# Performance work log

Hardware: AMD Instinct MI355X
Metric: run time of the kernel (lower is better)

## Reference

```python
import jax, jax.numpy as jnp
import numpy as np
import math

N = 100000
E = 1600000
D = 256          # input_size
H = 64           # head_size = input_size // n_heads = 256 // 4


def setup_inputs() -> dict:
    key = jax.random.key(0)
    k1, k2, k3, k4, k5 = jax.random.split(key, 5)
    X = jax.random.normal(k1, (N, D), dtype=jnp.float32)
    edge_index = jax.random.randint(k2, (2, E), 0, N, dtype=jnp.int64)
    # Linear(input_size, head_size, bias=False) weights, stored as [D, H] so Q = X @ Wq
    s = 1.0 / math.sqrt(D)
    Wq = jax.random.uniform(k3, (D, H), dtype=jnp.float32, minval=-s, maxval=s)
    Wk = jax.random.uniform(k4, (D, H), dtype=jnp.float32, minval=-s, maxval=s)
    Wv = jax.random.uniform(k5, (D, H), dtype=jnp.float32, minval=-s, maxval=s)
    return {"X": X, "Wq": Wq, "Wk": Wk, "Wv": Wv, "edge_index": edge_index}


def reference(X, Wq, Wk, Wv, edge_index):
    dk = math.sqrt(H)
    Q = X @ Wq  # [N, H]
    K = X @ Wk
    V = X @ Wv
    src = edge_index[0]  # row of sparse matrix -> softmax segment (dim=1 softmax)
    dst = edge_index[1]  # column -> neighbor supplying K/V
    scores = jnp.sum(Q[src] * K[dst], axis=-1) / dk  # [E]
    # per-row (per src node) stable softmax over edges
    m = jax.ops.segment_max(scores, src, num_segments=N)          # [N], -inf for empty rows
    m = jnp.where(jnp.isfinite(m), m, 0.0)
    e = jnp.exp(scores - m[src])                                   # [E]
    denom = jax.ops.segment_sum(e, src, num_segments=N)            # [N]
    alpha = e / jnp.maximum(denom[src], 1e-38)                     # [E]
    # scatter-weighted V aggregation: out[i] = sum_{(i,j) in edges} alpha_ij * V[j]
    out = jax.ops.segment_sum(alpha[:, None] * V[dst], src, num_segments=N)  # [N, H]
    return out
```

## Files before the change

### kernel.cpp

```cpp
#include <hip/hip_runtime.h>

typedef unsigned short u16;
typedef unsigned int u32;
typedef short short8 __attribute__((ext_vector_type(8)));
typedef float f32x4 __attribute__((ext_vector_type(4)));
typedef u32 u32x4 __attribute__((ext_vector_type(4)));

__device__ __forceinline__ u16 f2bf(float f) {
    union { float f; u32 i; } c; c.f = f;
    u32 i = c.i;
    return (u16)((i + 0x7FFFu + ((i >> 16) & 1u)) >> 16);
}
__device__ __forceinline__ float bf2f(u16 u) {
    union { u32 i; float f; } c; c.i = ((u32)u) << 16; return c.f;
}
__device__ __forceinline__ void bf2x(u32 p, float& lo, float& hi) {
    union { u32 i; float f; } a, b;
    a.i = p << 16; b.i = p & 0xFFFF0000u;
    lo = a.f; hi = b.f;
}
__device__ __forceinline__ u32 cvtpk_bf16(float lo, float hi) {
    u32 r;
    asm("v_cvt_pk_bf16_f32 %0, %1, %2" : "=v"(r) : "v"(lo), "v"(hi));
    return r;
}

__global__ void wfrag_kernel(const float* __restrict__ Wq,
                             const float* __restrict__ Wk,
                             const float* __restrict__ Wv,
                             u16* __restrict__ wf)
{
    int idx = blockIdx.x * 256 + threadIdx.x;
    if (idx >= 12 * 8 * 64) return;
    int lane = idx & 63;
    int s = (idx >> 6) & 7;
    int t = idx >> 9;
    int n = t * 16 + (lane & 15);
    const float* Wsrc = (n < 64) ? Wq : ((n < 128) ? Wk : Wv);
    int col = n & 63;
    int kbase = s * 32 + (lane >> 4) * 8;
    u16 o[8];
#pragma unroll
    for (int j = 0; j < 8; ++j) o[j] = f2bf(Wsrc[(size_t)(kbase + j) * 64 + col]);
    *(short8*)(wf + (size_t)idx * 8) = *(const short8*)o;
}

#define TM 32
__global__ __launch_bounds__(256, 2) void qkv_mfma(
    const float* __restrict__ X, const u16* __restrict__ wf,
    float* __restrict__ Qs, u16* __restrict__ KVsb,
    int N, int NT)
{
    __shared__ float xs[TM * 256];

    const int tid  = threadIdx.x;
    const int lane = tid & 63;
    const int wave = tid >> 6;
    const int m    = lane & 15;
    const int quad = lane >> 4;
    const int t0   = wave * 3;

    const short8* wfp = (const short8*)wf;
    short8 bfr0[8], bfr1[8], bfr2[8];
#pragma unroll
    for (int s = 0; s < 8; ++s) {
        bfr0[s] = wfp[(size_t)((t0 + 0) * 8 + s) * 64 + lane];
        bfr1[s] = wfp[(size_t)((t0 + 1) * 8 + s) * 64 + lane];
        bfr2[s] = wfp[(size_t)((t0 + 2) * 8 + s) * 64 + lane];
    }

    for (int tile = blockIdx.x; tile < NT; tile += gridDim.x) {
#pragma unroll
        for (int it = 0; it < 8; ++it) {
            int c0  = (it * 4 + wave) * 64;
            int c   = c0 + lane;
            int row = c >> 6;
            int sblk = (c & 63) ^ (row & 7);
            int arow = tile * TM + row;
            if (arow >= N) arow = N - 1;
            const float* g = X + (size_t)arow * 256 + sblk * 4;
            float* l = xs + c0 * 4;
            __builtin_amdgcn_global_load_lds(
                (const __attribute__((address_space(1))) void*)g,
                (__attribute__((address_space(3))) void*)l, 16, 0, 0);
        }
        __syncthreads();

        f32x4 acc[2][3];
#pragma unroll
        for (int rb = 0; rb < 2; ++rb)
#pragma unroll
            for (int tt = 0; tt < 3; ++tt) acc[rb][tt] = (f32x4)0.f;

#pragma unroll
        for (int rb = 0; rb < 2; ++rb) {
            const int row = rb * 16 + m;
            const float* xrow = xs + row * 256;
            const int sw = m & 7;
#pragma unroll
            for (int s = 0; s < 8; ++s) {
                int B0 = quad * 2 + s * 8;
                float4 a0 = *(const float4*)(xrow + ((B0)     ^ sw) * 4);
                float4 a1 = *(const float4*)(xrow + ((B0 + 1) ^ sw) * 4);
                union { u32x4 u; short8 s8; } af;
                af.u.x = cvtpk_bf16(a0.x, a0.y);
                af.u.y = cvtpk_bf16(a0.z, a0.w);
                af.u.z = cvtpk_bf16(a1.x, a1.y);
                af.u.w = cvtpk_bf16(a1.z, a1.w);
                acc[rb][0] = __builtin_amdgcn_mfma_f32_16x16x32_bf16(af.s8, bfr0[s], acc[rb][0], 0, 0, 0);
                acc[rb][1] = __builtin_amdgcn_mfma_f32_16x16x32_bf16(af.s8, bfr1[s], acc[rb][1], 0, 0, 0);
                acc[rb][2] = __builtin_amdgcn_mfma_f32_16x16x32_bf16(af.s8, bfr2[s], acc[rb][2], 0, 0, 0);
            }
        }

#pragma unroll
        for (int rb = 0; rb < 2; ++rb) {
            int rbase = tile * TM + rb * 16 + quad * 4;
#pragma unroll
            for (int tt = 0; tt < 3; ++tt) {
                int t = t0 + tt;
                int col = (t & 3) * 16 + m;
#pragma unroll
                for (int r = 0; r < 4; ++r) {
                    int rr = rbase + r;
                    if (rr >= N) continue;
                    float v = acc[rb][tt][r];
                    if (t < 4)      Qs  [(size_t)rr * 64  + col]      = v;
                    else if (t < 8) KVsb[(size_t)rr * 128 + col]      = f2bf(v);
                    else            KVsb[(size_t)rr * 128 + 64 + col] = f2bf(v);
                }
            }
        }
        __syncthreads();
    }
}


__global__ __launch_bounds__(256) void count_kernel(
    const int* __restrict__ src, int* __restrict__ bsize,
    int E, int N, int NB, int chunk)
{
    __shared__ int cnt[512];
    for (int i = threadIdx.x; i < 512; i += 256) cnt[i] = 0;
    __syncthreads();
    int lo = blockIdx.x * chunk;
    int hi = min(E, lo + chunk);
    for (int e = lo + (int)threadIdx.x; e < hi; e += 256) {
        int s = src[e];
        if ((unsigned)s < (unsigned)N) atomicAdd(&cnt[s >> 8], 1);
    }
    __syncthreads();
    for (int b = threadIdx.x; b < NB; b += 256)
        if (cnt[b]) atomicAdd(&bsize[b], cnt[b]);
}

__global__ __launch_bounds__(512) void scan391_kernel(
    const int* __restrict__ bsize, int* __restrict__ bbase,
    int* __restrict__ cursor, int* __restrict__ row_ptr_N, int NB)
{
    __shared__ int sd[512];
    int t = threadIdx.x;
    int v = (t < NB) ? bsize[t] : 0;
    sd[t] = v;
    __syncthreads();
    for (int off = 1; off < 512; off <<= 1) {
        int x = (t >= off) ? sd[t - off] : 0;
        __syncthreads();
        sd[t] += x;
        __syncthreads();
    }
    if (t < NB) {
        int excl = sd[t] - v;
        bbase[t] = excl;
        cursor[t] = excl;
        if (t == NB - 1) {
            bbase[NB] = sd[t];
            *row_ptr_N = sd[t];
        }
    }
}

__global__ __launch_bounds__(256) void scatter_pairs_kernel(
    const int* __restrict__ src, const int* __restrict__ dst,
    int* __restrict__ cursor, int2* __restrict__ pairs,
    int E, int N, int NB, int chunk)
{
    __shared__ int cnt[512];
    __shared__ int basei[512];
    for (int i = threadIdx.x; i < 512; i += 256) cnt[i] = 0;
    __syncthreads();
    int lo = blockIdx.x * chunk;
    int hi = min(E, lo + chunk);
    for (int e = lo + (int)threadIdx.x; e < hi; e += 256) {
        int s = src[e];
        if ((unsigned)s < (unsigned)N) atomicAdd(&cnt[s >> 8], 1);
    }
    __syncthreads();
    for (int b = threadIdx.x; b < NB; b += 256)
        basei[b] = cnt[b] ? atomicAdd(&cursor[b], cnt[b]) : 0;
    __syncthreads();
    for (int i = threadIdx.x; i < 512; i += 256) cnt[i] = 0;
    __syncthreads();
    for (int e = lo + (int)threadIdx.x; e < hi; e += 256) {
        int s = src[e];
        if ((unsigned)s >= (unsigned)N) continue;
        int d = dst[e];
        if ((unsigned)d >= (unsigned)N) d = 0;
        int bk = s >> 8;
        int p = basei[bk] + atomicAdd(&cnt[bk], 1);
        pairs[p] = make_int2(s, d);
    }
}

#define MAXB 6144
__global__ __launch_bounds__(256) void sort_bucket_kernel(
    const int2* __restrict__ pairs, const int* __restrict__ bbase,
    int* __restrict__ row_ptr, int* __restrict__ sorted_dst, int N)
{
    __shared__ int deg[256];
    __shared__ int off[256];
    __shared__ int cur[256];
    __shared__ int ldst[MAXB];

    int bk = blockIdx.x;
    int n0 = bk * 256;
    int nn = min(256, N - n0);
    int base = bbase[bk];
    int size = bbase[bk + 1] - base;
    int t = threadIdx.x;

    deg[t] = 0;
    __syncthreads();
    for (int i = t; i < size; i += 256)
        atomicAdd(&deg[pairs[base + i].x & 255], 1);
    __syncthreads();
    off[t] = deg[t];
    __syncthreads();
    for (int s = 1; s < 256; s <<= 1) {
        int x = (t >= s) ? off[t - s] : 0;
        __syncthreads();
        off[t] += x;
        __syncthreads();
    }
    int excl = off[t] - deg[t];
    cur[t] = excl;
    if (t < nn) row_ptr[n0 + t] = base + excl;
    __syncthreads();
    int cap = min(size, MAXB);
    for (int i = t; i < size; i += 256) {
        int2 pr = pairs[base + i];
        int p = atomicAdd(&cur[pr.x & 255], 1);
        if (p < MAXB) ldst[p] = pr.y;
    }
    __syncthreads();
    for (int i = t; i < cap; i += 256)
        sorted_dst[base + i] = ldst[i];
    for (int i = cap + t; i < size; i += 256)
        sorted_dst[base + i] = 0;
}

__global__ __launch_bounds__(256) void attn_csr(
    const float* __restrict__ Qs, const u16* __restrict__ KVsb,
    const int* __restrict__ row_ptr, const int* __restrict__ sdst,
    float* __restrict__ out, int N)
{
    int sg = (int)((blockIdx.x * 256 + threadIdx.x) >> 3);
    if (sg >= N) return;
    int sl = threadIdx.x & 7;

    const float* qp = Qs + (size_t)sg * 64 + sl * 8;
    float4 q0 = *(const float4*)(qp);
    float4 q1 = *(const float4*)(qp + 4);

    int beg = row_ptr[sg];
    int end = row_ptr[sg + 1];

    float l = 0.f;
    float a0 = 0.f, a1 = 0.f, a2 = 0.f, a3 = 0.f;
    float a4 = 0.f, a5 = 0.f, a6 = 0.f, a7 = 0.f;

    if (beg < end) {
        int d0 = sdst[beg];
        const u16* kv = KVsb + (size_t)d0 * 128 + sl * 8;
        uint4 kr = *(const uint4*)(kv);
        uint4 vr = *(const uint4*)(kv + 64);

        for (int j = beg; j < end; ++j) {
            int jn = j + 1;
            int dn = (jn < end) ? sdst[jn] : d0;
            const u16* kvn = KVsb + (size_t)dn * 128 + sl * 8;
            uint4 krn = *(const uint4*)(kvn);
            uint4 vrn = *(const uint4*)(kvn + 64);

            float k0, k1, k2, k3, k4, k5, k6, k7;
            bf2x(kr.x, k0, k1); bf2x(kr.y, k2, k3);
            bf2x(kr.z, k4, k5); bf2x(kr.w, k6, k7);

            float p = q0.x * k0 + q0.y * k1 + q0.z * k2 + q0.w * k3
                    + q1.x * k4 + q1.y * k5 + q1.z * k6 + q1.w * k7;
            p += __shfl_xor(p, 1);
            p += __shfl_xor(p, 2);
            p += __shfl_xor(p, 4);

            float pe = __expf(p * 0.125f);

            float v0, v1, v2, v3, v4, v5, v6, v7;
            bf2x(vr.x, v0, v1); bf2x(vr.y, v2, v3);
            bf2x(vr.z, v4, v5); bf2x(vr.w, v6, v7);

            l += pe;
            a0 += pe * v0; a1 += pe * v1; a2 += pe * v2; a3 += pe * v3;
            a4 += pe * v4; a5 += pe * v5; a6 += pe * v6; a7 += pe * v7;

            kr = krn; vr = vrn;
        }
    }

    float inv = (l > 0.f) ? (1.f / l) : 0.f;
    float* op = out + (size_t)sg * 64 + sl * 8;
    *(float4*)(op)     = make_float4(a0 * inv, a1 * inv, a2 * inv, a3 * inv);
    *(float4*)(op + 4) = make_float4(a4 * inv, a5 * inv, a6 * inv, a7 * inv);
}

extern "C" void kernel_launch(void* const* d_in, const int* in_sizes, int n_in,
                              void* d_out, int out_size, void* d_ws, size_t ws_size,
                              hipStream_t stream)
{
    const float* X  = (const float*)d_in[0];
    const float* Wq = (const float*)d_in[1];
    const float* Wk = (const float*)d_in[2];
    const float* Wv = (const float*)d_in[3];
    const int*   ei = (const int*)d_in[4];

    const int N = in_sizes[0] / 256;
    const int E = in_sizes[4] / 2;
    const int* src = ei;
    const int* dst = ei + E;
    const int NB = (N + 255) >> 8;

    char* w = (char*)d_ws;
    float* Qs = (float*)w;      w += (size_t)N * 64 * sizeof(float);
    u16* KVsb = (u16*)w;        w += (size_t)N * 128 * sizeof(u16);
    int2* pairs = (int2*)w;     w += (size_t)E * sizeof(int2);
    int* sorted_dst = (int*)w;  w += (size_t)E * sizeof(int);
    int* row_ptr = (int*)w;     w += (size_t)(N + 1) * sizeof(int);
    int* bsize = (int*)w;       w += (size_t)(NB + 1) * sizeof(int);
    int* bbase = (int*)w;       w += (size_t)(NB + 1) * sizeof(int);
    int* cursor = (int*)w;      w += (size_t)(NB + 1) * sizeof(int);
    u16* wf = (u16*)w;          w += (size_t)12 * 8 * 64 * 8 * sizeof(u16);

    hipMemsetAsync(bsize, 0, (size_t)(NB + 1) * sizeof(int), stream);

    const int B1 = 160;
    const int chunk = (E + B1 - 1) / B1;
    const int NT = (N + TM - 1) / TM;

    wfrag_kernel<<<24, 256, 0, stream>>>(Wq, Wk, Wv, wf);
    qkv_mfma<<<768, 256, 0, stream>>>(X, wf, Qs, KVsb, N, NT);

    count_kernel<<<B1, 256, 0, stream>>>(src, bsize, E, N, NB, chunk);
    scan391_kernel<<<1, 512, 0, stream>>>(bsize, bbase, cursor, row_ptr + N, NB);
    scatter_pairs_kernel<<<B1, 256, 0, stream>>>(src, dst, cursor, pairs, E, N, NB, chunk);
    sort_bucket_kernel<<<NB, 256, 0, stream>>>(pairs, bbase, row_ptr, sorted_dst, N);

    attn_csr<<<(N * 8 + 255) / 256, 256, 0, stream>>>(
        Qs, KVsb, row_ptr, sorted_dst, (float*)d_out, N);
}
```

Before: 337.8 us.

## Deepen gather prefetch in edge aggregation loop to four in-flight K/V rows

Replaces the single-stage prefetch of the next neighbor's K/V row with a 4-deep register ring, plus a further-ahead prefetch of destination indices. The goal is more memory-level parallelism, hiding the latency of random gathers in the attention aggregation loop. The cost is more registers and wasted loads and exp work on padded tail edges, which are masked out of the accumulation.

```diff
diff --git a/kernel.cpp b/kernel.cpp
--- a/kernel.cpp
+++ b/kernel.cpp
@@ -280,39 +280,57 @@
     float a4 = 0.f, a5 = 0.f, a6 = 0.f, a7 = 0.f;
 
     if (beg < end) {
-        int d0 = sdst[beg];
-        const u16* kv = KVsb + (size_t)d0 * 128 + sl * 8;
-        uint4 kr = *(const uint4*)(kv);
-        uint4 vr = *(const uint4*)(kv + 64);
-
-        for (int j = beg; j < end; ++j) {
-            int jn = j + 1;
-            int dn = (jn < end) ? sdst[jn] : d0;
-            const u16* kvn = KVsb + (size_t)dn * 128 + sl * 8;
-            uint4 krn = *(const uint4*)(kvn);
-            uint4 vrn = *(const uint4*)(kvn + 64);
-
-            float k0, k1, k2, k3, k4, k5, k6, k7;
-            bf2x(kr.x, k0, k1); bf2x(kr.y, k2, k3);
-            bf2x(kr.z, k4, k5); bf2x(kr.w, k6, k7);
-
-            float p = q0.x * k0 + q0.y * k1 + q0.z * k2 + q0.w * k3
-                    + q1.x * k4 + q1.y * k5 + q1.z * k6 + q1.w * k7;
-            p += __shfl_xor(p, 1);
-            p += __shfl_xor(p, 2);
-            p += __shfl_xor(p, 4);
-
-            float pe = __expf(p * 0.125f);
-
-            float v0, v1, v2, v3, v4, v5, v6, v7;
-            bf2x(vr.x, v0, v1); bf2x(vr.y, v2, v3);
-            bf2x(vr.z, v4, v5); bf2x(vr.w, v6, v7);
-
-            l += pe;
-            a0 += pe * v0; a1 += pe * v1; a2 += pe * v2; a3 += pe * v3;
-            a4 += pe * v4; a5 += pe * v5; a6 += pe * v6; a7 += pe * v7;
-
-            kr = krn; vr = vrn;
+        const int last = end - 1;
+        uint4 kr[4], vr[4];
+        int pd[4];
+
+#pragma unroll
+        for (int i = 0; i < 4; ++i) {
+            int e = beg + i;
+            int d = sdst[e <= last ? e : last];
+            const u16* kv = KVsb + (size_t)d * 128 + sl * 8;
+            kr[i] = *(const uint4*)(kv);
+            vr[i] = *(const uint4*)(kv + 64);
+            int ep = beg + 4 + i;
+            pd[i] = sdst[ep <= last ? ep : last];
+        }
+
+        for (int base = beg; base < end; base += 4) {
+#pragma unroll
+            for (int i = 0; i < 4; ++i) {
+                int e = base + i;
+                uint4 k = kr[i], v = vr[i];
+
+                {
+                    const u16* kv = KVsb + (size_t)pd[i] * 128 + sl * 8;
+                    kr[i] = *(const uint4*)(kv);
+                    vr[i] = *(const uint4*)(kv + 64);
+                    int ep = e + 8;
+                    pd[i] = sdst[ep <= last ? ep : last];
+                }
+
+                float k0, k1, k2, k3, k4, k5, k6, k7;
+                bf2x(k.x, k0, k1); bf2x(k.y, k2, k3);
+                bf2x(k.z, k4, k5); bf2x(k.w, k6, k7);
+
+                float p = q0.x * k0 + q0.y * k1 + q0.z * k2 + q0.w * k3
+                        + q1.x * k4 + q1.y * k5 + q1.z * k6 + q1.w * k7;
+                p += __shfl_xor(p, 1);
+                p += __shfl_xor(p, 2);
+                p += __shfl_xor(p, 4);
+
+                float pe = __expf(p * 0.125f);
+
+                float v0, v1, v2, v3, v4, v5, v6, v7;
+                bf2x(v.x, v0, v1); bf2x(v.y, v2, v3);
+                bf2x(v.z, v4, v5); bf2x(v.w, v6, v7);
+
+                if (e < end) {
+                    l += pe;
+                    a0 += pe * v0; a1 += pe * v1; a2 += pe * v2; a3 += pe * v3;
+                    a4 += pe * v4; a5 += pe * v5; a6 += pe * v6; a7 += pe * v7;
+                }
+            }
         }
     }
 
```

After: 330.4 us. -2.2%, faster.
